# Kernel tuning notes

Hardware: AMD Instinct MI355X
Metric: run time of the kernel (lower is better)

The kernel has to match this reference:

```python
import jax, jax.numpy as jnp
import numpy as np

B, C, N = 8, 256, 2048
H = max(1, C // 8)  # hidden = in_channels // 8 = 32


def setup_inputs() -> dict:
    key = jax.random.key(0)
    ks = jax.random.split(key, 7)
    s = 0.05
    return {
        "x": jax.random.normal(ks[0], (B, C, N), dtype=jnp.float32),
        "wq": jax.random.normal(ks[1], (H, C), dtype=jnp.float32) * s,
        "bq": jax.random.normal(ks[2], (H,), dtype=jnp.float32) * s,
        "wk": jax.random.normal(ks[3], (H, C), dtype=jnp.float32) * s,
        "bk": jax.random.normal(ks[4], (H,), dtype=jnp.float32) * s,
        "wv": jax.random.normal(ks[5], (C, C), dtype=jnp.float32) * s,
        "bv": jax.random.normal(ks[6], (C,), dtype=jnp.float32) * s,
    }


def reference(x, wq, bq, wk, bk, wv, bv):
    # 1x1 Conv1d == per-position linear: weight [out, in]
    q = jnp.einsum('bcn,hc->bnh', x, wq) + bq                  # [B, N, H] (already permuted)
    k = jnp.einsum('bcn,hc->bhn', x, wk) + bk[None, :, None]   # [B, H, N]
    v = jnp.einsum('bcn,dc->bdn', x, wv) + bv[None, :, None]   # [B, C, N]
    energy = jnp.einsum('bnh,bhm->bnm', q, k)                  # [B, N, N] (no scaling, as in source)
    weights = jax.nn.softmax(energy, axis=-1)                  # softmax over last dim
    # out = bmm(value, weights^T): out[b,c,i] = sum_j v[b,c,j] * weights[b,i,j]
    out = jnp.einsum('bcj,bij->bci', v, weights)               # [B, C, N]
    return out + x
```

## Files before the change

### kernel.cpp

```cpp
#include <hip/hip_runtime.h>
#include <hip/hip_bf16.h>
#include <cstdint>
#include <cstddef>

#define B_ 8
#define C_ 256
#define N_ 2048
#define H_ 32

typedef __bf16 bf8 __attribute__((ext_vector_type(8)));
typedef float f4 __attribute__((ext_vector_type(4)));
typedef float f16v __attribute__((ext_vector_type(16)));

__device__ inline void gload_lds16(const void* g, void* l) {
  __builtin_amdgcn_global_load_lds(
      (const __attribute__((address_space(1))) unsigned int*)g,
      (__attribute__((address_space(3))) unsigned int*)l, 16, 0, 0);
}

__global__ __launch_bounds__(256) void pack_kernel(
    const float* __restrict__ wq, const float* __restrict__ wk,
    const float* __restrict__ wv, const float* __restrict__ bq,
    const float* __restrict__ bk, const float* __restrict__ bv,
    __hip_bfloat16* __restrict__ wpk, float* __restrict__ bpk) {
  int r = blockIdx.x, c = threadIdx.x;
  float v;
  if (r < 256)      v = wv[r * 256 + c];
  else if (r < 288) v = wq[(r - 256) * 256 + c];
  else              v = wk[(r - 288) * 256 + c];
  wpk[r * 256 + c] = __float2bfloat16(v);
  if (c == 0) bpk[r] = (r < 256) ? bv[r] : (r < 288 ? bq[r - 256] : bk[r - 288]);
}

__global__ __launch_bounds__(256) void proj_kernel(
    const float* __restrict__ x, const __hip_bfloat16* __restrict__ wpk,
    const float* __restrict__ bpk, __hip_bfloat16* __restrict__ vbf,
    __hip_bfloat16* __restrict__ qkb) {
  __shared__ __attribute__((aligned(16))) __hip_bfloat16 As[320 * 32];
  int tid = threadIdx.x, wv = tid >> 6, lane = tid & 63;
  int b = blockIdx.y;
  int n0 = blockIdx.x * 32;
  int fcol = lane & 15, hi4 = lane >> 4;
  int grow = lane >> 2, gc = (lane & 3) * 8;
  const float* xb = x + (size_t)b * C_ * N_;
  f4 acc[5][2] = {};
  for (int k0 = 0; k0 < C_; k0 += 32) {
    __syncthreads();
#pragma unroll
    for (int g = 0; g < 5; ++g)
      gload_lds16(wpk + (size_t)(wv * 80 + g * 16 + grow) * 256 + k0 + gc,
                  &As[(wv * 80 + g * 16) * 32]);
    bf8 bfr[2];
#pragma unroll
    for (int j = 0; j < 2; ++j) {
      int n = n0 + j * 16 + fcol;
      float tmp[8];
#pragma unroll
      for (int e = 0; e < 8; ++e)
        tmp[e] = xb[(size_t)(k0 + hi4 * 8 + e) * N_ + n];
#pragma unroll
      for (int e = 0; e < 8; ++e) bfr[j][e] = (__bf16)tmp[e];
    }
    __syncthreads();
#pragma unroll
    for (int s = 0; s < 5; ++s) {
      bf8 af = *(const bf8*)&As[(wv * 80 + s * 16 + fcol) * 32 + hi4 * 8];
      acc[s][0] = __builtin_amdgcn_mfma_f32_16x16x32_bf16(af, bfr[0], acc[s][0], 0, 0, 0);
      acc[s][1] = __builtin_amdgcn_mfma_f32_16x16x32_bf16(af, bfr[1], acc[s][1], 0, 0, 0);
    }
  }
  int rq = hi4 * 4;
#pragma unroll
  for (int s = 0; s < 5; ++s)
#pragma unroll
    for (int r = 0; r < 4; ++r) {
      int m = wv * 80 + s * 16 + rq + r;
      float bias = bpk[m];
#pragma unroll
      for (int j = 0; j < 2; ++j) {
        int n = n0 + j * 16 + fcol;
        float val = acc[s][j][r] + bias;
        if (m < 256)
          vbf[((size_t)b * C_ + m) * N_ + n] = __float2bfloat16(val);
        else
          qkb[((size_t)b * N_ + n) * 64 + (m - 256)] = __float2bfloat16(val);
      }
    }
}

#define FJT 64

__global__ __launch_bounds__(256, 2) void fused_attn(
    const __hip_bfloat16* __restrict__ qk,
    const __hip_bfloat16* __restrict__ vbf,
    const float* __restrict__ x, float* __restrict__ out) {
  __shared__ __attribute__((aligned(16))) __hip_bfloat16 vS[2][128 * FJT];
  __shared__ __attribute__((aligned(16))) __hip_bfloat16 pS[2][2][32 * 72];
  __shared__ float lSp[2][2][32];
  int tid = threadIdx.x;
  int wv = tid >> 6, lane = tid & 63;
  int iw = wv >> 1, cw = wv & 1;
  int b = blockIdx.z;
  int c0 = blockIdx.x * 128;
  int i0 = blockIdx.y * 64;
  int l31 = lane & 31, hi = lane >> 5;

  const __hip_bfloat16* qkB = qk + (size_t)b * N_ * 64;
  bf8 qf0 = *(const bf8*)&qkB[(size_t)(i0 + iw * 32 + l31) * 64 + hi * 8];
  bf8 qf1 = *(const bf8*)&qkB[(size_t)(i0 + iw * 32 + l31) * 64 + 16 + hi * 8];

  const __hip_bfloat16* vB = vbf + ((size_t)b * C_ + c0) * N_;
  int grow = lane >> 3;
  int gch = ((lane & 7) ^ (grow & 7)) * 8;
  int kjrow = cw * 32 + l31;

  bf8 kf0, kf1, kn0, kn1;
#pragma unroll
  for (int g = 0; g < 4; ++g)
    gload_lds16(vB + (size_t)(wv * 32 + g * 8 + grow) * N_ + gch,
                &vS[0][(wv * 32 + g * 8) * FJT]);
  kf0 = *(const bf8*)&qkB[(size_t)kjrow * 64 + 32 + hi * 8];
  kf1 = *(const bf8*)&qkB[(size_t)kjrow * 64 + 32 + 16 + hi * 8];

  f16v acc0 = {}, acc1 = {};
  float lp[16];
#pragma unroll
  for (int r = 0; r < 16; ++r) lp[r] = 0.f;

  for (int t = 0; t < N_ / FJT; ++t) {
    int buf = t & 1;
    f16v s = {};
    s = __builtin_amdgcn_mfma_f32_32x32x16_bf16(qf0, kf0, s, 0, 0, 0);
    s = __builtin_amdgcn_mfma_f32_32x32x16_bf16(qf1, kf1, s, 0, 0, 0);
    __hip_bfloat16* pW = &pS[buf][iw][0];
#pragma unroll
    for (int r = 0; r < 16; ++r) {
      float p = __expf(s[r]);
      lp[r] += p;
      int row = (r & 3) + 8 * (r >> 2) + 4 * hi;
      pW[row * 72 + cw * 32 + l31] = __float2bfloat16(p);
    }
    __syncthreads();
    if (t + 1 < N_ / FJT) {
      int j1 = (t + 1) * FJT;
#pragma unroll
      for (int g = 0; g < 4; ++g)
        gload_lds16(vB + (size_t)(wv * 32 + g * 8 + grow) * N_ + j1 + gch,
                    &vS[buf ^ 1][(wv * 32 + g * 8) * FJT]);
      kn0 = *(const bf8*)&qkB[(size_t)(j1 + kjrow) * 64 + 32 + hi * 8];
      kn1 = *(const bf8*)&qkB[(size_t)(j1 + kjrow) * 64 + 32 + 16 + hi * 8];
    }
    const __hip_bfloat16* pR = &pS[buf][iw][0];
    int r0 = cw * 64 + l31, r1 = r0 + 32;
    int sw = r0 & 7;
#pragma unroll
    for (int jc = 0; jc < 4; ++jc) {
      int ch = jc * 2 + hi;
      bf8 pf = *(const bf8*)&pR[l31 * 72 + jc * 16 + hi * 8];
      bf8 vf0 = *(const bf8*)&vS[buf][r0 * FJT + ((ch ^ sw) * 8)];
      bf8 vf1 = *(const bf8*)&vS[buf][r1 * FJT + ((ch ^ sw) * 8)];
      acc0 = __builtin_amdgcn_mfma_f32_32x32x16_bf16(vf0, pf, acc0, 0, 0, 0);
      acc1 = __builtin_amdgcn_mfma_f32_32x32x16_bf16(vf1, pf, acc1, 0, 0, 0);
    }
    if (t + 1 < N_ / FJT) { kf0 = kn0; kf1 = kn1; }
  }

#pragma unroll
  for (int r = 0; r < 16; ++r) {
    float v = lp[r];
    v += __shfl_xor(v, 1); v += __shfl_xor(v, 2); v += __shfl_xor(v, 4);
    v += __shfl_xor(v, 8); v += __shfl_xor(v, 16);
    lp[r] = v;
  }
  if (l31 == 0) {
#pragma unroll
    for (int r = 0; r < 16; ++r)
      lSp[iw][cw][(r & 3) + 8 * (r >> 2) + 4 * hi] = lp[r];
  }
  __syncthreads();
  float linv = 1.0f / (lSp[iw][0][l31] + lSp[iw][1][l31]);
  int i = i0 + iw * 32 + l31;
  const float* xr = x + (size_t)b * C_ * N_;
  float* op = out + (size_t)b * C_ * N_;
#pragma unroll
  for (int r = 0; r < 16; ++r) {
    int row = (r & 3) + 8 * (r >> 2) + 4 * hi;
    size_t o0 = (size_t)(c0 + cw * 64 + row) * N_ + i;
    op[o0] = acc0[r] * linv + xr[o0];
    size_t o1 = o0 + (size_t)32 * N_;
    op[o1] = acc1[r] * linv + xr[o1];
  }
}

extern "C" void kernel_launch(void* const* d_in, const int* in_sizes, int n_in,
                              void* d_out, int out_size, void* d_ws, size_t ws_size,
                              hipStream_t stream) {
  const float* x  = (const float*)d_in[0];
  const float* wq = (const float*)d_in[1];
  const float* bq = (const float*)d_in[2];
  const float* wk = (const float*)d_in[3];
  const float* bk = (const float*)d_in[4];
  const float* wv = (const float*)d_in[5];
  const float* bv = (const float*)d_in[6];
  float* out = (float*)d_out;

  char* ws = (char*)d_ws;
  __hip_bfloat16* qkb = (__hip_bfloat16*)ws;
  __hip_bfloat16* vbf = (__hip_bfloat16*)(ws + (2u << 20));
  __hip_bfloat16* wpk = (__hip_bfloat16*)(ws + (10u << 20));
  float*          bpk = (float*)(ws + (10u << 20) + (256u << 10));

  pack_kernel<<<dim3(320), 256, 0, stream>>>(wq, wk, wv, bq, bk, bv, wpk, bpk);
  proj_kernel<<<dim3(N_ / 32, B_), 256, 0, stream>>>(x, wpk, bpk, vbf, qkb);
  fused_attn<<<dim3(C_ / 128, N_ / 64, B_), 256, 0, stream>>>(qkb, vbf, x, out);
}
```

Measured before the change: 137.8 us.

## Double-buffer projection weight tiles and remap attention blocks batch-major across XCDs

The projection kernel now double-buffers its LDS weight tiles and prefetches the next x slice into registers, which overlaps global loads with MFMA work and removes one barrier per k-step. The attention kernel uses a flattened 1D grid where the low bits select the batch. With round-robin XCD dispatch, each XCD then works on a single batch's K/V data, which should improve L2 locality. The cost is doubled LDS in the projection kernel and higher register pressure from the prefetch buffers.

New measurement: 134.9 us. 1.02x faster.

```diff
diff --git a/kernel.cpp b/kernel.cpp
--- a/kernel.cpp
+++ b/kernel.cpp
@@ -36,35 +36,52 @@
     const float* __restrict__ x, const __hip_bfloat16* __restrict__ wpk,
     const float* __restrict__ bpk, __hip_bfloat16* __restrict__ vbf,
     __hip_bfloat16* __restrict__ qkb) {
-  __shared__ __attribute__((aligned(16))) __hip_bfloat16 As[320 * 32];
+  __shared__ __attribute__((aligned(16))) __hip_bfloat16 As[2][320 * 32];
   int tid = threadIdx.x, wv = tid >> 6, lane = tid & 63;
   int b = blockIdx.y;
   int n0 = blockIdx.x * 32;
   int fcol = lane & 15, hi4 = lane >> 4;
   int grow = lane >> 2, gc = (lane & 3) * 8;
   const float* xb = x + (size_t)b * C_ * N_;
+
+#pragma unroll
+  for (int g = 0; g < 5; ++g)
+    gload_lds16(wpk + (size_t)(wv * 80 + g * 16 + grow) * 256 + gc,
+                &As[0][(wv * 80 + g * 16) * 32]);
+  float xr[2][8];
+#pragma unroll
+  for (int j = 0; j < 2; ++j)
+#pragma unroll
+    for (int e = 0; e < 8; ++e)
+      xr[j][e] = xb[(size_t)(hi4 * 8 + e) * N_ + n0 + j * 16 + fcol];
+
   f4 acc[5][2] = {};
-  for (int k0 = 0; k0 < C_; k0 += 32) {
+  for (int t = 0; t < 8; ++t) {
+    int buf = t & 1;
     __syncthreads();
-#pragma unroll
-    for (int g = 0; g < 5; ++g)
-      gload_lds16(wpk + (size_t)(wv * 80 + g * 16 + grow) * 256 + k0 + gc,
-                  &As[(wv * 80 + g * 16) * 32]);
+    if (t < 7) {
+      int k1 = (t + 1) * 32;
+#pragma unroll
+      for (int g = 0; g < 5; ++g)
+        gload_lds16(wpk + (size_t)(wv * 80 + g * 16 + grow) * 256 + k1 + gc,
+                    &As[buf ^ 1][(wv * 80 + g * 16) * 32]);
+    }
     bf8 bfr[2];
 #pragma unroll
-    for (int j = 0; j < 2; ++j) {
-      int n = n0 + j * 16 + fcol;
-      float tmp[8];
-#pragma unroll
-      for (int e = 0; e < 8; ++e)
-        tmp[e] = xb[(size_t)(k0 + hi4 * 8 + e) * N_ + n];
-#pragma unroll
-      for (int e = 0; e < 8; ++e) bfr[j][e] = (__bf16)tmp[e];
-    }
-    __syncthreads();
+    for (int j = 0; j < 2; ++j)
+#pragma unroll
+      for (int e = 0; e < 8; ++e) bfr[j][e] = (__bf16)xr[j][e];
+    if (t < 7) {
+      int k1 = (t + 1) * 32;
+#pragma unroll
+      for (int j = 0; j < 2; ++j)
+#pragma unroll
+        for (int e = 0; e < 8; ++e)
+          xr[j][e] = xb[(size_t)(k1 + hi4 * 8 + e) * N_ + n0 + j * 16 + fcol];
+    }
 #pragma unroll
     for (int s = 0; s < 5; ++s) {
-      bf8 af = *(const bf8*)&As[(wv * 80 + s * 16 + fcol) * 32 + hi4 * 8];
+      bf8 af = *(const bf8*)&As[buf][(wv * 80 + s * 16 + fcol) * 32 + hi4 * 8];
       acc[s][0] = __builtin_amdgcn_mfma_f32_16x16x32_bf16(af, bfr[0], acc[s][0], 0, 0, 0);
       acc[s][1] = __builtin_amdgcn_mfma_f32_16x16x32_bf16(af, bfr[1], acc[s][1], 0, 0, 0);
     }
@@ -100,9 +117,11 @@
   int tid = threadIdx.x;
   int wv = tid >> 6, lane = tid & 63;
   int iw = wv >> 1, cw = wv & 1;
-  int b = blockIdx.z;
-  int c0 = blockIdx.x * 128;
-  int i0 = blockIdx.y * 64;
+  int blk = blockIdx.x;
+  int b = blk & 7;
+  int rest = blk >> 3;
+  int c0 = (rest & 1) * 128;
+  int i0 = (rest >> 1) * 64;
   int l31 = lane & 31, hi = lane >> 5;
 
   const __hip_bfloat16* qkB = qk + (size_t)b * N_ * 64;
@@ -212,5 +231,5 @@
 
   pack_kernel<<<dim3(320), 256, 0, stream>>>(wq, wk, wv, bq, bk, bv, wpk, bpk);
   proj_kernel<<<dim3(N_ / 32, B_), 256, 0, stream>>>(x, wpk, bpk, vbf, qkb);
-  fused_attn<<<dim3(C_ / 128, N_ / 64, B_), 256, 0, stream>>>(qkb, vbf, x, out);
-}
+  fused_attn<<<dim3(512), 256, 0, stream>>>(qkb, vbf, x, out);
+}
```
